# Performance work log

Hardware: AMD Instinct MI355X
Metric: run time of the kernel (lower is better)

Reference implementation:

```python
import jax, jax.numpy as jnp
import numpy as np
from jax import lax

B, BANDS, HW = 128, 30, 15
DIM, NH, NC = 512, 8, 16
EPS = 1e-5

def _ln(x, w, b):
    m = x.mean(-1, keepdims=True)
    v = ((x - m) ** 2).mean(-1, keepdims=True)
    return (x - m) / jnp.sqrt(v + EPS) * w + b

def _bn(x, g, b, m, v):
    # eval-mode BatchNorm2d over NCHW
    inv = g / jnp.sqrt(v + EPS)
    return x * inv[None, :, None, None] + (b - m * inv)[None, :, None, None]

def _conv(x, w, b):
    y = lax.conv_general_dilated(x, w, (1, 1), 'SAME', dimension_numbers=('NCHW', 'OIHW', 'NCHW'))
    return y + b[None, :, None, None]

def _attn(x, qkv_w, qkv_b, proj_w, proj_b):
    Bq, N, C = x.shape
    hd = C // NH
    qkv = (x @ qkv_w.T + qkv_b).reshape(Bq, N, 3, NH, hd).transpose(2, 0, 3, 1, 4)
    q, k, v = qkv[0], qkv[1], qkv[2]
    a = jax.nn.softmax(jnp.einsum('bhnd,bhmd->bhnm', q, k) * (hd ** -0.5), axis=-1)
    o = jnp.einsum('bhnm,bhmd->bhnd', a, v).transpose(0, 2, 1, 3).reshape(Bq, N, C)
    return o @ proj_w.T + proj_b

def _mlp(x, w1, b1, w2, b2):
    return jax.nn.gelu(x @ w1.T + b1, approximate=False) @ w2.T + b2

def _forward(x, conv_h_w, conv_h_b, bn_h_g, bn_h_b, bn_h_m, bn_h_v, cnn_conv_w, cnn_conv_b, cnn_bn_g, cnn_bn_b, cnn_bn_m, cnn_bn_v, cnn_fc_w, cnn_fc_b, spa_cls, spe_cls, spa_pos, spe_pos, blk_n1_w, blk_n1_b, blk_n2_w, blk_n2_b, blk_qkv_w, blk_qkv_b, blk_proj_w, blk_proj_b, blk_fc1_w, blk_fc1_b, blk_fc2_w, blk_fc2_b, norm1_w, norm1_b, norm2_w, norm2_b, head_w, head_b):
    x = x[:, 0]  # squeeze(1) -> [B, BANDS, H, W]
    Bn = x.shape[0]
    # --- spatial stream ---
    h = jax.nn.relu(_bn(_conv(x, conv_h_w, conv_h_b), bn_h_g, bn_h_b, bn_h_m, bn_h_v))
    spa = h.reshape(Bn, DIM, -1).transpose(0, 2, 1)  # b (h w) c
    spa = jnp.concatenate([jnp.broadcast_to(spa_cls, (Bn, 1, DIM)), spa], axis=1) + spa_pos
    # --- spectral stream: per-band CNN batched across bands in one pass ---
    bands = x.reshape(Bn * BANDS, 1, HW, HW)
    f = jax.nn.relu(_bn(_conv(bands, cnn_conv_w, cnn_conv_b), cnn_bn_g, cnn_bn_b, cnn_bn_m, cnn_bn_v))
    f = f.mean(axis=(2, 3))  # adaptive avg pool to 1x1
    f = jax.nn.relu(f @ cnn_fc_w.T + cnn_fc_b).reshape(Bn, BANDS, DIM)
    spe = jnp.concatenate([jnp.broadcast_to(spe_cls, (Bn, 1, DIM)), f], axis=1) + spe_pos
    xs, ys = spa, spe
    for i in range(2):  # CTMF blocks (eval: drop_path/dropout are identity)
        xin = _ln(jnp.concatenate([ys[:, :1], xs[:, 1:]], axis=1), blk_n1_w[i], blk_n1_b[i])
        yin = _ln(jnp.concatenate([xs[:, :1], ys[:, 1:]], axis=1), blk_n1_w[i], blk_n1_b[i])
        x_ = _attn(xin, blk_qkv_w[i], blk_qkv_b[i], blk_proj_w[i], blk_proj_b[i])
        y_ = _attn(yin, blk_qkv_w[i], blk_qkv_b[i], blk_proj_w[i], blk_proj_b[i])
        xs2 = xs + jnp.concatenate([xs[:, :1] + y_[:, :1], x_[:, 1:]], axis=1)
        ys2 = ys + jnp.concatenate([ys[:, :1] + x_[:, :1], y_[:, 1:]], axis=1)
        xs = xs2 + _mlp(_ln(xs2, blk_n2_w[i], blk_n2_b[i]), blk_fc1_w[i], blk_fc1_b[i], blk_fc2_w[i], blk_fc2_b[i])
        ys = ys2 + _mlp(_ln(ys2, blk_n2_w[i], blk_n2_b[i]), blk_fc1_w[i], blk_fc1_b[i], blk_fc2_w[i], blk_fc2_b[i])
    cls = jnp.concatenate([_ln(xs[:, 0], norm1_w, norm1_b), _ln(ys[:, 0], norm2_w, norm2_b)], axis=-1)
    return cls @ head_w.T + head_b

def setup_inputs() -> dict:
    key = jax.random.key(0)
    ks = jax.random.split(key, 32)
    r = lambda i, shape, s=0.02: jax.random.normal(ks[i], shape, dtype=jnp.float32) * s
    Nspa = HW * HW + 1
    Nspe = BANDS + 1
    return {
        'x': jax.random.normal(ks[0], (B, 1, BANDS, HW, HW), dtype=jnp.float32),
        'conv_h_w': r(1, (DIM, BANDS, 3, 3)),
        'conv_h_b': jnp.zeros((DIM,), jnp.float32),
        'bn_h_g': 1.0 + r(2, (DIM,)),
        'bn_h_b': r(3, (DIM,)),
        'bn_h_m': r(4, (DIM,), 0.1),
        'bn_h_v': 0.5 + jax.random.uniform(ks[5], (DIM,), dtype=jnp.float32),
        'cnn_conv_w': r(6, (128, 1, 3, 3), 0.1),
        'cnn_conv_b': jnp.zeros((128,), jnp.float32),
        'cnn_bn_g': 1.0 + r(7, (128,)),
        'cnn_bn_b': r(8, (128,)),
        'cnn_bn_m': r(9, (128,), 0.1),
        'cnn_bn_v': 0.5 + jax.random.uniform(ks[10], (128,), dtype=jnp.float32),
        'cnn_fc_w': r(11, (DIM, 128)),
        'cnn_fc_b': jnp.zeros((DIM,), jnp.float32),
        'spa_cls': jnp.zeros((1, 1, DIM), jnp.float32),
        'spe_cls': jnp.zeros((1, 1, DIM), jnp.float32),
        'spa_pos': r(12, (1, Nspa, DIM)),
        'spe_pos': r(13, (1, Nspe, DIM)),
        'blk_n1_w': jnp.ones((2, DIM), jnp.float32),
        'blk_n1_b': jnp.zeros((2, DIM), jnp.float32),
        'blk_n2_w': jnp.ones((2, DIM), jnp.float32),
        'blk_n2_b': jnp.zeros((2, DIM), jnp.float32),
        'blk_qkv_w': r(14, (2, 3 * DIM, DIM)),
        'blk_qkv_b': jnp.zeros((2, 3 * DIM), jnp.float32),
        'blk_proj_w': r(15, (2, DIM, DIM)),
        'blk_proj_b': jnp.zeros((2, DIM), jnp.float32),
        'blk_fc1_w': r(16, (2, DIM, DIM)),
        'blk_fc1_b': jnp.zeros((2, DIM), jnp.float32),
        'blk_fc2_w': r(17, (2, DIM, DIM)),
        'blk_fc2_b': jnp.zeros((2, DIM), jnp.float32),
        'norm1_w': jnp.ones((DIM,), jnp.float32),
        'norm1_b': jnp.zeros((DIM,), jnp.float32),
        'norm2_w': jnp.ones((DIM,), jnp.float32),
        'norm2_b': jnp.zeros((DIM,), jnp.float32),
        'head_w': r(18, (NC, 2 * DIM)),
        'head_b': jnp.zeros((NC,), jnp.float32),
    }

def reference(x, conv_h_w, conv_h_b, bn_h_g, bn_h_b, bn_h_m, bn_h_v, cnn_conv_w, cnn_conv_b, cnn_bn_g, cnn_bn_b, cnn_bn_m, cnn_bn_v, cnn_fc_w, cnn_fc_b, spa_cls, spe_cls, spa_pos, spe_pos, blk_n1_w, blk_n1_b, blk_n2_w, blk_n2_b, blk_qkv_w, blk_qkv_b, blk_proj_w, blk_proj_b, blk_fc1_w, blk_fc1_b, blk_fc2_w, blk_fc2_b, norm1_w, norm1_b, norm2_w, norm2_b, head_w, head_b):
    return _forward(x, conv_h_w, conv_h_b, bn_h_g, bn_h_b, bn_h_m, bn_h_v, cnn_conv_w, cnn_conv_b, cnn_bn_g, cnn_bn_b, cnn_bn_m, cnn_bn_v, cnn_fc_w, cnn_fc_b, spa_cls, spe_cls, spa_pos, spe_pos, blk_n1_w, blk_n1_b, blk_n2_w, blk_n2_b, blk_qkv_w, blk_qkv_b, blk_proj_w, blk_proj_b, blk_fc1_w, blk_fc1_b, blk_fc2_w, blk_fc2_b, norm1_w, norm1_b, norm2_w, norm2_b, head_w, head_b)
```

## Files before the change

### kernel.cpp

```cpp
#include <hip/hip_runtime.h>
#include <hip/hip_bf16.h>

typedef unsigned short u16;
typedef __attribute__((ext_vector_type(8))) short bf16x8;
typedef __attribute__((ext_vector_type(4))) float f32x4;

#define NB 128
#define BANDS 30
#define HWD 15
#define NPIX 225
#define DIMC 512
#define NHEAD 8
#define HD 64
#define NSPA 226
#define NSPE 31
#define EPSF 1e-5f
#define KCONV 320
#define MXROWS 28928
#define MYROWS 3968
#define M2ROWS 32896

__device__ __forceinline__ float b2f(u16 u) { return __uint_as_float(((unsigned)u) << 16); }
__device__ __forceinline__ u16 f2b(float f) {
  __hip_bfloat16 h = __float2bfloat16(f);
  return *reinterpret_cast<u16*>(&h);
}

#if __has_builtin(__builtin_amdgcn_global_load_lds)
#define HAVE_GLDS 1
__device__ __forceinline__ void gl_lds16(const void* g, void* l) {
  __builtin_amdgcn_global_load_lds((const __attribute__((address_space(1))) void*)g,
                                   (__attribute__((address_space(3))) void*)l, 16, 0, 0);
}
#else
#define HAVE_GLDS 0
#endif

__global__ __launch_bounds__(256) void cvt_k(const float* __restrict__ s, u16* __restrict__ d, int n) {
  for (int i = blockIdx.x * 256 + threadIdx.x; i < n; i += gridDim.x * 256) d[i] = f2b(s[i]);
}

__global__ __launch_bounds__(256) void convw_k(const float* __restrict__ w, u16* __restrict__ d) {
  int i = blockIdx.x * 256 + threadIdx.x;
  if (i >= DIMC * KCONV) return;
  int r = i / KCONV, c = i - r * KCONV;
  d[i] = (c < 270) ? f2b(w[r * 270 + c]) : (u16)0;
}

__global__ __launch_bounds__(256) void bnprep_k(const float* __restrict__ g, const float* __restrict__ bb,
    const float* __restrict__ bm, const float* __restrict__ bv, const float* __restrict__ cb,
    float* __restrict__ sc, float* __restrict__ sh) {
  int n = blockIdx.x * 256 + threadIdx.x;
  if (n < DIMC) {
    float inv = g[n] * rsqrtf(bv[n] + EPSF);
    sc[n] = inv;
    sh[n] = (cb[n] - bm[n]) * inv + bb[n];
  }
}

__global__ __launch_bounds__(256) void im2col_k(const float* __restrict__ x, u16* __restrict__ Ac) {
  int idx = blockIdx.x * 256 + threadIdx.x;
  if (idx >= 28800 * 40) return;
  int m = idx / 40, g = idx - m * 40;
  int b = m / NPIX, p = m - b * NPIX;
  int i = p / 15, j = p - i * 15;
  union { u16 v[8]; uint4 u; } out;
#pragma unroll
  for (int e = 0; e < 8; e++) {
    int c = g * 8 + e;
    float v = 0.f;
    if (c < 270) {
      int band = c / 9, q = c - band * 9;
      int di = q / 3, dj = q - di * 3;
      int ii = i + di - 1, jj = j + dj - 1;
      if ((unsigned)ii < 15u && (unsigned)jj < 15u)
        v = x[((size_t)b * BANDS + band) * NPIX + ii * 15 + jj];
    }
    out.v[e] = f2b(v);
  }
  *reinterpret_cast<uint4*>(Ac + (size_t)m * KCONV + g * 8) = out.u;
}

__global__ __launch_bounds__(256) void cls_init_k(const float* __restrict__ spa_cls,
    const float* __restrict__ spe_cls, const float* __restrict__ spa_pos,
    const float* __restrict__ spe_pos, float* __restrict__ xs, float* __restrict__ ys) {
  int b = blockIdx.x, t = threadIdx.x;
  int d0 = t, d1 = t + 256;
  xs[(size_t)b * NSPA * DIMC + d0] = spa_cls[d0] + spa_pos[d0];
  xs[(size_t)b * NSPA * DIMC + d1] = spa_cls[d1] + spa_pos[d1];
  ys[(size_t)b * NSPE * DIMC + d0] = spe_cls[d0] + spe_pos[d0];
  ys[(size_t)b * NSPE * DIMC + d1] = spe_cls[d1] + spe_pos[d1];
}

__global__ __launch_bounds__(256) void cnn_conv_k(const float* __restrict__ x,
    const float* __restrict__ w, const float* __restrict__ cb, const float* __restrict__ g,
    const float* __restrict__ bb, const float* __restrict__ bm, const float* __restrict__ bv,
    u16* __restrict__ pooled) {
  __shared__ float img[2][NPIX];
  int b0 = blockIdx.x * 2;
  int t = threadIdx.x;
  for (int idx = t; idx < 2 * NPIX; idx += 256) ((float*)img)[idx] = x[(size_t)b0 * NPIX + idx];
  __syncthreads();
  int half = t >> 7, ch = t & 127;
  const float* im = img[half];
  float inv = g[ch] * rsqrtf(bv[ch] + EPSF);
  float beta = bb[ch] - bm[ch] * inv;
  float w9[9];
#pragma unroll
  for (int q = 0; q < 9; q++) w9[q] = w[ch * 9 + q] * inv;
  float bias = cb[ch] * inv + beta;

  float rm[15], rc[15], rp[15];
#pragma unroll
  for (int j = 0; j < 15; j++) { rm[j] = 0.f; rc[j] = im[j]; }
  float sum = 0.f;
  for (int i = 0; i < 15; i++) {
#pragma unroll
    for (int j = 0; j < 15; j++) rp[j] = (i < 14) ? im[(i + 1) * 15 + j] : 0.f;
    float a[15];
#pragma unroll
    for (int j = 0; j < 15; j++) a[j] = fmaf(w9[4], rc[j], bias);
#pragma unroll
    for (int j = 0; j < 15; j++) {
      if (j > 0)  a[j] = fmaf(w9[3], rc[j - 1], a[j]);
      if (j < 14) a[j] = fmaf(w9[5], rc[j + 1], a[j]);
      a[j] = fmaf(w9[1], rm[j], a[j]);
      if (j > 0)  a[j] = fmaf(w9[0], rm[j - 1], a[j]);
      if (j < 14) a[j] = fmaf(w9[2], rm[j + 1], a[j]);
      a[j] = fmaf(w9[7], rp[j], a[j]);
      if (j > 0)  a[j] = fmaf(w9[6], rp[j - 1], a[j]);
      if (j < 14) a[j] = fmaf(w9[8], rp[j + 1], a[j]);
    }
#pragma unroll
    for (int j = 0; j < 15; j++) sum += fmaxf(a[j], 0.f);
#pragma unroll
    for (int j = 0; j < 15; j++) { rm[j] = rc[j]; rc[j] = rp[j]; }
  }
  pooled[(size_t)(b0 + half) * 128 + ch] = f2b(sum * (1.0f / 225.0f));
}

template <int GATHER>
__global__ __launch_bounds__(256) void ln_c_k(const float* __restrict__ xsc,
    const float* __restrict__ w, const float* __restrict__ bprm, u16* __restrict__ out) {
  int row = blockIdx.x;
  const float* src;
  if (GATHER) {
    if (row < MXROWS) {
      int b = row / NSPA, tk = row - b * NSPA;
      src = (tk == 0) ? xsc + ((size_t)MXROWS + (size_t)b * NSPE) * DIMC
                      : xsc + (size_t)row * DIMC;
    } else {
      int ry = row - MXROWS;
      int b = ry / NSPE, tk = ry - b * NSPE;
      src = (tk == 0) ? xsc + (size_t)b * NSPA * DIMC : xsc + (size_t)row * DIMC;
    }
  } else {
    src = xsc + (size_t)row * DIMC;
  }
  int t = threadIdx.x;
  float x0 = src[t], x1 = src[t + 256];
  float s = x0 + x1, sq = x0 * x0 + x1 * x1;
  for (int off = 32; off; off >>= 1) { s += __shfl_down(s, off); sq += __shfl_down(sq, off); }
  __shared__ float sa[4], sb4[4];
  int wid = t >> 6;
  if ((t & 63) == 0) { sa[wid] = s; sb4[wid] = sq; }
  __syncthreads();
  s = sa[0] + sa[1] + sa[2] + sa[3];
  sq = sb4[0] + sb4[1] + sb4[2] + sb4[3];
  float mean = s * (1.0f / 512.0f);
  float var = sq * (1.0f / 512.0f) - mean * mean;
  float rstd = rsqrtf(var + EPSF);
  out[(size_t)row * DIMC + t] = f2b((x0 - mean) * rstd * w[t] + bprm[t]);
  out[(size_t)row * DIMC + t + 256] = f2b((x1 - mean) * rstd * w[t + 256] + bprm[t + 256]);
}

__global__ __launch_bounds__(256) void ln_cls_k(const float* __restrict__ xs,
    const float* __restrict__ ys, const float* __restrict__ w1, const float* __restrict__ b1,
    const float* __restrict__ w2, const float* __restrict__ b2, float* __restrict__ cls) {
  int gb = blockIdx.x;
  int half = gb & 1, b = gb >> 1;
  const float* src = half ? (ys + (size_t)b * NSPE * DIMC) : (xs + (size_t)b * NSPA * DIMC);
  const float* w = half ? w2 : w1;
  const float* bp = half ? b2 : b1;
  int t = threadIdx.x;
  float x0 = src[t], x1 = src[t + 256];
  float s = x0 + x1, sq = x0 * x0 + x1 * x1;
  for (int off = 32; off; off >>= 1) { s += __shfl_down(s, off); sq += __shfl_down(sq, off); }
  __shared__ float sa[4], sb4[4];
  int wid = t >> 6;
  if ((t & 63) == 0) { sa[wid] = s; sb4[wid] = sq; }
  __syncthreads();
  s = sa[0] + sa[1] + sa[2] + sa[3];
  sq = sb4[0] + sb4[1] + sb4[2] + sb4[3];
  float mean = s * (1.0f / 512.0f);
  float var = sq * (1.0f / 512.0f) - mean * mean;
  float rstd = rsqrtf(var + EPSF);
  cls[(size_t)b * 1024 + half * DIMC + t] = (x0 - mean) * rstd * w[t] + bp[t];
  cls[(size_t)b * 1024 + half * DIMC + t + 256] = (x1 - mean) * rstd * w[t + 256] + bp[t + 256];
}

template <int MODE>
__global__ __launch_bounds__(256) void mgemm_k(const u16* __restrict__ A, const u16* __restrict__ Bw,
    const float* __restrict__ bias, float* outf, u16* outb, int M, int N, int K,
    const float* aux0, const float* aux1, const float* aux2) {
  __shared__ u16 As[128 * 64];
  __shared__ u16 Bs[128 * 64];
  const int t = threadIdx.x;
  const int wid = t >> 6, l = t & 63;
  const int wm = wid >> 1, wn = wid & 1;
  const int fr = l & 15, kg = l >> 4;

  const int nx = gridDim.x, nwg = nx * gridDim.y;
  int hlin = blockIdx.y * nx + blockIdx.x;
  int xcd = hlin & 7, j = hlin >> 3;
  int q8 = nwg >> 3, r8 = nwg & 7;
  int L = (xcd < r8 ? xcd * (q8 + 1) : r8 * (q8 + 1) + (xcd - r8) * q8) + j;
  const int n0 = (L % nx) * 128, m0 = (L / nx) * 128;

  const int srow = l >> 3;
  const int sslot = l & 7;

  f32x4 acc[4][4];
#pragma unroll
  for (int i = 0; i < 4; i++)
#pragma unroll
    for (int j2 = 0; j2 < 4; j2++) acc[i][j2] = (f32x4){0.f, 0.f, 0.f, 0.f};

  for (int kq = 0; kq < K; kq += 64) {
#if !HAVE_GLDS
    uint4 ra[4], rb[4];
#pragma unroll
    for (int i = 0; i < 4; i++) {
      int r = wid * 32 + i * 8 + srow;
      int cg = sslot ^ (r & 7);
      ra[i] = *reinterpret_cast<const uint4*>(A + (size_t)(m0 + r) * K + kq + cg * 8);
      rb[i] = *reinterpret_cast<const uint4*>(Bw + (size_t)(n0 + r) * K + kq + cg * 8);
    }
#endif
    __syncthreads();
#if HAVE_GLDS
#pragma unroll
    for (int i = 0; i < 4; i++) {
      int r = wid * 32 + i * 8 + srow;
      int cg = sslot ^ (r & 7);
      gl_lds16(A + (size_t)(m0 + r) * K + kq + cg * 8, &As[(wid * 32 + i * 8) * 64]);
      gl_lds16(Bw + (size_t)(n0 + r) * K + kq + cg * 8, &Bs[(wid * 32 + i * 8) * 64]);
    }
#else
#pragma unroll
    for (int i = 0; i < 4; i++) {
      int r = wid * 32 + i * 8 + srow;
      *reinterpret_cast<uint4*>(&As[r * 64 + sslot * 8]) = ra[i];
      *reinterpret_cast<uint4*>(&Bs[r * 64 + sslot * 8]) = rb[i];
    }
#endif
    __syncthreads();
#pragma unroll
    for (int h = 0; h < 2; h++) {
      bf16x8 af[4], bfr[4];
#pragma unroll
      for (int mi = 0; mi < 4; mi++) {
        int r = wm * 64 + mi * 16 + fr;
        af[mi] = *reinterpret_cast<const bf16x8*>(&As[r * 64 + (((h * 4 + kg) ^ (fr & 7)) * 8)]);
      }
#pragma unroll
      for (int nj = 0; nj < 4; nj++) {
        int n = wn * 64 + nj * 16 + fr;
        bfr[nj] = *reinterpret_cast<const bf16x8*>(&Bs[n * 64 + (((h * 4 + kg) ^ (fr & 7)) * 8)]);
      }
#pragma unroll
      for (int mi = 0; mi < 4; mi++)
#pragma unroll
        for (int nj = 0; nj < 4; nj++)
          acc[mi][nj] = __builtin_amdgcn_mfma_f32_16x16x32_bf16(af[mi], bfr[nj], acc[mi][nj], 0, 0, 0);
    }
  }

#pragma unroll
  for (int mi = 0; mi < 4; mi++) {
#pragma unroll
    for (int q = 0; q < 4; q++) {
      int m = m0 + wm * 64 + mi * 16 + kg * 4 + q;
#pragma unroll
      for (int nj = 0; nj < 4; nj++) {
        int n = n0 + wn * 64 + nj * 16 + fr;
        float v = acc[mi][nj][q];
        if (MODE == 0) {
          outb[(size_t)m * N + n] = f2b(v + bias[n]);
        } else if (MODE == 1) {
          float z = v + bias[n];
          outb[(size_t)m * N + n] = f2b(0.5f * z * (1.0f + erff(z * 0.70710678118f)));
        } else if (MODE == 2) {
          size_t idx = (size_t)m * N + n;
          outf[idx] = v + bias[n] + aux0[idx];
        } else if (MODE == 3) {
          int b = m / NPIX, p = m - b * NPIX;
          float z = fmaxf(v * aux0[n] + aux1[n], 0.f) + aux2[(size_t)(p + 1) * DIMC + n];
          outf[((size_t)b * NSPA + p + 1) * DIMC + n] = z;
        } else if (MODE == 4) {
          int b = m / BANDS, band = m - b * BANDS;
          float z = fmaxf(v + bias[n], 0.f) + aux0[(size_t)(band + 1) * DIMC + n];
          outf[((size_t)b * NSPE + band + 1) * DIMC + n] = z;
        } else if (MODE == 5) {
          float z = v + bias[n];
          int tk, sidx;
          if (m < MXROWS) {
            int b = m / NSPA; tk = m - b * NSPA; sidx = b;
          } else {
            int ry = m - MXROWS; int b = ry / NSPE; tk = ry - b * NSPE; sidx = 128 + b;
          }
          if (tk == 0) outb[(size_t)sidx * DIMC + n] = f2b(z);
          else outf[(size_t)m * N + n] += z;
        }
      }
    }
  }
}

__global__ __launch_bounds__(256) void cls_swap_k(float* __restrict__ xsc,
                                                  const u16* __restrict__ clsprj) {
  int b = blockIdx.x, t = threadIdx.x;
  size_t xrow = (size_t)b * NSPA * DIMC;
  size_t yrow = ((size_t)MXROWS + (size_t)b * NSPE) * DIMC;
#pragma unroll
  for (int q = 0; q < 2; q++) {
    int d = t + q * 256;
    xsc[xrow + d] = 2.0f * xsc[xrow + d] + b2f(clsprj[(size_t)(128 + b) * DIMC + d]);
    xsc[yrow + d] = 2.0f * xsc[yrow + d] + b2f(clsprj[(size_t)b * DIMC + d]);
  }
}

template <int NTOK, int KP>
__global__ __launch_bounds__(256) void vt_k(const u16* __restrict__ qkv, u16* __restrict__ vtout) {
  __shared__ u16 Vl[64 * 72];
  int h = blockIdx.x, b = blockIdx.y;
  int t = threadIdx.x;
  const size_t rs = 3 * DIMC;
  const u16* src = qkv + (size_t)b * NTOK * rs + 2 * DIMC + h * HD;
  u16* dst = vtout + (size_t)(b * NHEAD + h) * HD * KP;
  for (int kt = 0; kt < KP / 64; kt++) {
    __syncthreads();
#pragma unroll
    for (int p = 0; p < 2; p++) {
      int idx = p * 256 + t;
      int row = idx >> 3, c = idx & 7;
      int tok = kt * 64 + row;
      uint4 v = make_uint4(0, 0, 0, 0);
      if (tok < NTOK) v = *reinterpret_cast<const uint4*>(src + (size_t)tok * rs + c * 8);
      *reinterpret_cast<uint4*>(&Vl[row * 72 + c * 8]) = v;
    }
    __syncthreads();
    int d = t & 63, tg = t >> 6;
    unsigned pu[8];
#pragma unroll
    for (int i = 0; i < 8; i++) {
      unsigned a = Vl[(tg * 16 + 2 * i) * 72 + d];
      unsigned bb2 = Vl[(tg * 16 + 2 * i + 1) * 72 + d];
      pu[i] = (bb2 << 16) | a;
    }
    uint4 o0 = make_uint4(pu[0], pu[1], pu[2], pu[3]);
    uint4 o1 = make_uint4(pu[4], pu[5], pu[6], pu[7]);
    u16* dp = dst + (size_t)d * KP + kt * 64 + tg * 16;
    *reinterpret_cast<uint4*>(dp) = o0;
    *reinterpret_cast<uint4*>(dp + 8) = o1;
  }
}

__device__ __forceinline__ int fsw(int row, int chunk) {
  return row * 64 + ((chunk ^ (row & 7)) << 3);
}
__device__ __forceinline__ void stage64(const u16* __restrict__ gsrc, size_t gstride,
                                        u16* lds, int w, int l) {
#pragma unroll
  for (int i = 0; i < 2; i++) {
    int r = w * 16 + i * 8 + (l >> 3);
    int c = l & 7;
    int scg = c ^ (r & 7);
    const u16* g = gsrc + (size_t)r * gstride + scg * 8;
#if HAVE_GLDS
    gl_lds16(g, &lds[(w * 16 + i * 8) * 64]);
#else
    *reinterpret_cast<uint4*>(&lds[r * 64 + c * 8]) = *reinterpret_cast<const uint4*>(g);
#endif
  }
}

__global__ __launch_bounds__(256) void flashm_k(const u16* __restrict__ qkv,
    const u16* __restrict__ vt, u16* __restrict__ o, int N, int kpad, float scale) {
  __shared__ u16 Qs[64 * 64], Ks[64 * 64], Vs[64 * 64];
  __shared__ u16 Ol[64 * 72];
  const int qt = blockIdx.x, h = blockIdx.y, b = blockIdx.z;
  const int t = threadIdx.x;
  const int w = t >> 6, l = t & 63;
  const int lr = l & 15, lk = l >> 4;
  const size_t rs = 3 * DIMC;
  const size_t qbase = (size_t)b * N * rs + h * HD;
  const u16* vbase = vt + (size_t)(b * NHEAD + h) * HD * kpad;

  stage64(qkv + qbase + (size_t)(qt * 64) * rs, rs, Qs, w, l);
  __syncthreads();
  bf16x8 bq0 = *reinterpret_cast<const bf16x8*>(&Qs[fsw(w * 16 + lr, lk)]);
  bf16x8 bq1 = *reinterpret_cast<const bf16x8*>(&Qs[fsw(w * 16 + lr, 4 + lk)]);

  float m_i = -1e30f, l_i = 0.f;
  f32x4 oacc[4];
#pragma unroll
  for (int mi = 0; mi < 4; mi++) oacc[mi] = (f32x4){0.f, 0.f, 0.f, 0.f};

  const int nkt = (kpad + 63) >> 6;
  for (int kt = 0; kt < nkt; kt++) {
    __syncthreads();
    stage64(qkv + qbase + DIMC + (size_t)(kt * 64) * rs, rs, Ks, w, l);
    stage64(vbase + kt * 64, (size_t)kpad, Vs, w, l);
    __syncthreads();

    f32x4 st[4];
#pragma unroll
    for (int mi = 0; mi < 4; mi++) st[mi] = (f32x4){0.f, 0.f, 0.f, 0.f};
#pragma unroll
    for (int mi = 0; mi < 4; mi++) {
      bf16x8 ak0 = *reinterpret_cast<const bf16x8*>(&Ks[fsw(mi * 16 + lr, lk)]);
      bf16x8 ak1 = *reinterpret_cast<const bf16x8*>(&Ks[fsw(mi * 16 + lr, 4 + lk)]);
      st[mi] = __builtin_amdgcn_mfma_f32_16x16x32_bf16(ak0, bq0, st[mi], 0, 0, 0);
      st[mi] = __builtin_amdgcn_mfma_f32_16x16x32_bf16(ak1, bq1, st[mi], 0, 0, 0);
    }

    float sv[4][4];
    float tmax = -1e30f;
#pragma unroll
    for (int mi = 0; mi < 4; mi++)
#pragma unroll
      for (int q = 0; q < 4; q++) {
        int kgl = kt * 64 + mi * 16 + lk * 4 + q;
        float v = (kgl < N) ? st[mi][q] * scale : -1e30f;
        sv[mi][q] = v;
        tmax = fmaxf(tmax, v);
      }
    tmax = fmaxf(tmax, __shfl_xor(tmax, 16));
    tmax = fmaxf(tmax, __shfl_xor(tmax, 32));
    float mn = fmaxf(m_i, tmax);
    float corr = __expf(m_i - mn);
    m_i = mn;
    float rsum = 0.f;
#pragma unroll
    for (int mi = 0; mi < 4; mi++)
#pragma unroll
      for (int q = 0; q < 4; q++) {
        float p = __expf(sv[mi][q] - mn);
        sv[mi][q] = p;
        rsum += p;
      }
    rsum += __shfl_xor(rsum, 16);
    rsum += __shfl_xor(rsum, 32);
    l_i = l_i * corr + rsum;
#pragma unroll
    for (int mi = 0; mi < 4; mi++) oacc[mi] *= corr;

    unsigned pk[4][2];
#pragma unroll
    for (int mi = 0; mi < 4; mi++) {
      pk[mi][0] = ((unsigned)f2b(sv[mi][1]) << 16) | (unsigned)f2b(sv[mi][0]);
      pk[mi][1] = ((unsigned)f2b(sv[mi][3]) << 16) | (unsigned)f2b(sv[mi][2]);
    }
    int src0 = lr + 32 * (lk & 1);
    int src1 = src0 + 16;
    bool hi = lk >= 2;
    bf16x8 pbv[2];
#pragma unroll
    for (int c = 0; c < 2; c++) {
      unsigned a0 = __shfl(pk[2 * c][0], src0), b0 = __shfl(pk[2 * c + 1][0], src0);
      unsigned a1 = __shfl(pk[2 * c][1], src0), b1 = __shfl(pk[2 * c + 1][1], src0);
      unsigned a2 = __shfl(pk[2 * c][0], src1), b2 = __shfl(pk[2 * c + 1][0], src1);
      unsigned a3 = __shfl(pk[2 * c][1], src1), b3 = __shfl(pk[2 * c + 1][1], src1);
      union { unsigned u[4]; bf16x8 v; } pu;
      pu.u[0] = hi ? b0 : a0;
      pu.u[1] = hi ? b1 : a1;
      pu.u[2] = hi ? b2 : a2;
      pu.u[3] = hi ? b3 : a3;
      pbv[c] = pu.v;
    }

#pragma unroll
    for (int mi = 0; mi < 4; mi++) {
      bf16x8 av0 = *reinterpret_cast<const bf16x8*>(&Vs[fsw(mi * 16 + lr, lk)]);
      bf16x8 av1 = *reinterpret_cast<const bf16x8*>(&Vs[fsw(mi * 16 + lr, 4 + lk)]);
      oacc[mi] = __builtin_amdgcn_mfma_f32_16x16x32_bf16(av0, pbv[0], oacc[mi], 0, 0, 0);
      oacc[mi] = __builtin_amdgcn_mfma_f32_16x16x32_bf16(av1, pbv[1], oacc[mi], 0, 0, 0);
    }
  }

  float invl = 1.0f / l_i;
#pragma unroll
  for (int mi = 0; mi < 4; mi++) {
    unsigned lo = ((unsigned)f2b(oacc[mi][1] * invl) << 16) | (unsigned)f2b(oacc[mi][0] * invl);
    unsigned hi2 = ((unsigned)f2b(oacc[mi][3] * invl) << 16) | (unsigned)f2b(oacc[mi][2] * invl);
    uint2 pr; pr.x = lo; pr.y = hi2;
    *reinterpret_cast<uint2*>(&Ol[(w * 16 + lr) * 72 + mi * 16 + lk * 4]) = pr;
  }
  __syncthreads();
  {
    int row = t >> 2, c4 = t & 3;
    int qrow = qt * 64 + row;
    if (qrow < N) {
      uint4 v0 = *reinterpret_cast<const uint4*>(&Ol[row * 72 + c4 * 8]);
      uint4 v1 = *reinterpret_cast<const uint4*>(&Ol[row * 72 + (c4 + 4) * 8]);
      u16* op = o + ((size_t)b * N + qrow) * DIMC + h * HD;
      *reinterpret_cast<uint4*>(op + c4 * 8) = v0;
      *reinterpret_cast<uint4*>(op + (c4 + 4) * 8) = v1;
    }
  }
}

__global__ __launch_bounds__(256) void head_k(const float* __restrict__ cls,
    const float* __restrict__ hw, const float* __restrict__ hb, float* __restrict__ out) {
  __shared__ float cl[1024];
  __shared__ float part[256];
  int b = blockIdx.x, t = threadIdx.x;
  for (int idx = t; idx < 1024; idx += 256) cl[idx] = cls[(size_t)b * 1024 + idx];
  __syncthreads();
  int c = t >> 4, sl = t & 15;
  float p = 0.f;
  for (int j = 0; j < 64; j++) p += cl[sl * 64 + j] * hw[(size_t)c * 1024 + sl * 64 + j];
  part[t] = p;
  __syncthreads();
  if (sl == 0) {
    float sum = hb[c];
    for (int q = 0; q < 16; q++) sum += part[c * 16 + q];
    out[(size_t)b * 16 + c] = sum;
  }
}

extern "C" void kernel_launch(void* const* d_in, const int* in_sizes, int n_in,
                              void* d_out, int out_size, void* d_ws, size_t ws_size,
                              hipStream_t stream) {
  const float* x        = (const float*)d_in[0];
  const float* conv_h_w = (const float*)d_in[1];
  const float* conv_h_b = (const float*)d_in[2];
  const float* bn_h_g   = (const float*)d_in[3];
  const float* bn_h_b   = (const float*)d_in[4];
  const float* bn_h_m   = (const float*)d_in[5];
  const float* bn_h_v   = (const float*)d_in[6];
  const float* cnn_conv_w = (const float*)d_in[7];
  const float* cnn_conv_b = (const float*)d_in[8];
  const float* cnn_bn_g = (const float*)d_in[9];
  const float* cnn_bn_b = (const float*)d_in[10];
  const float* cnn_bn_m = (const float*)d_in[11];
  const float* cnn_bn_v = (const float*)d_in[12];
  const float* cnn_fc_w = (const float*)d_in[13];
  const float* cnn_fc_b = (const float*)d_in[14];
  const float* spa_cls  = (const float*)d_in[15];
  const float* spe_cls  = (const float*)d_in[16];
  const float* spa_pos  = (const float*)d_in[17];
  const float* spe_pos  = (const float*)d_in[18];
  const float* blk_n1_w = (const float*)d_in[19];
  const float* blk_n1_b = (const float*)d_in[20];
  const float* blk_n2_w = (const float*)d_in[21];
  const float* blk_n2_b = (const float*)d_in[22];
  const float* blk_qkv_w = (const float*)d_in[23];
  const float* blk_qkv_b = (const float*)d_in[24];
  const float* blk_proj_w = (const float*)d_in[25];
  const float* blk_proj_b = (const float*)d_in[26];
  const float* blk_fc1_w = (const float*)d_in[27];
  const float* blk_fc1_b = (const float*)d_in[28];
  const float* blk_fc2_w = (const float*)d_in[29];
  const float* blk_fc2_b = (const float*)d_in[30];
  const float* norm1_w  = (const float*)d_in[31];
  const float* norm1_b  = (const float*)d_in[32];
  const float* norm2_w  = (const float*)d_in[33];
  const float* norm2_b  = (const float*)d_in[34];
  const float* head_w   = (const float*)d_in[35];
  const float* head_b   = (const float*)d_in[36];

  char* ws = (char*)d_ws;
  size_t off = 0;
  auto take = [&](size_t bytes) -> char* {
    char* p = ws + off;
    off = (off + bytes + 255) & ~(size_t)255;
    return p;
  };
  const int Mx = MXROWS, M2 = M2ROWS;
  const int Mc = NB * NPIX;
  const int Mf = NB * BANDS;
  float* xsc  = (float*)take((size_t)M2 * DIMC * 4);
  float* ysb  = xsc + (size_t)Mx * DIMC;
  u16* xyin   = (u16*)take((size_t)M2 * DIMC * 2);
  u16* qkvxy  = (u16*)take((size_t)M2 * 3 * DIMC * 2);
  u16* oxy    = (u16*)take((size_t)M2 * DIMC * 2);
  u16* clsprj = (u16*)take((size_t)256 * DIMC * 2);
  float* clsb = (float*)take((size_t)NB * 1024 * 4);
  u16* pooled = (u16*)take((size_t)Mf * 128 * 2);
  u16* qkvWb  = (u16*)take((size_t)2 * 3 * DIMC * DIMC * 2);
  u16* projWb = (u16*)take((size_t)2 * DIMC * DIMC * 2);
  u16* fc1Wb  = (u16*)take((size_t)2 * DIMC * DIMC * 2);
  u16* fc2Wb  = (u16*)take((size_t)2 * DIMC * DIMC * 2);
  u16* fcWb   = (u16*)take((size_t)DIMC * 128 * 2);
  u16* convWb = (u16*)take((size_t)DIMC * KCONV * 2);
  float* bnsc = (float*)take(DIMC * 4);
  float* bnsh = (float*)take(DIMC * 4);
  u16* vty    = (u16*)take((size_t)NB * NHEAD * HD * 64 * 2);
  u16* Acol   = qkvxy;
  u16* vtx    = xyin;

  cvt_k<<<1024, 256, 0, stream>>>(blk_qkv_w, qkvWb, 2 * 3 * DIMC * DIMC);
  cvt_k<<<1024, 256, 0, stream>>>(blk_proj_w, projWb, 2 * DIMC * DIMC);
  cvt_k<<<1024, 256, 0, stream>>>(blk_fc1_w, fc1Wb, 2 * DIMC * DIMC);
  cvt_k<<<1024, 256, 0, stream>>>(blk_fc2_w, fc2Wb, 2 * DIMC * DIMC);
  cvt_k<<<256, 256, 0, stream>>>(cnn_fc_w, fcWb, DIMC * 128);
  convw_k<<<(DIMC * KCONV + 255) / 256, 256, 0, stream>>>(conv_h_w, convWb);
  bnprep_k<<<2, 256, 0, stream>>>(bn_h_g, bn_h_b, bn_h_m, bn_h_v, conv_h_b, bnsc, bnsh);

  cls_init_k<<<NB, 256, 0, stream>>>(spa_cls, spe_cls, spa_pos, spe_pos, xsc, ysb);
  im2col_k<<<(Mc * 40 + 255) / 256, 256, 0, stream>>>(x, Acol);
  mgemm_k<3><<<dim3(4, Mc / 128), 256, 0, stream>>>(Acol, convWb, nullptr, xsc, nullptr,
      Mc, DIMC, KCONV, bnsc, bnsh, spa_pos);
  cnn_conv_k<<<Mf / 2, 256, 0, stream>>>(x, cnn_conv_w, cnn_conv_b, cnn_bn_g, cnn_bn_b,
                                         cnn_bn_m, cnn_bn_v, pooled);
  mgemm_k<4><<<dim3(4, Mf / 128), 256, 0, stream>>>(pooled, fcWb, cnn_fc_b, ysb, nullptr,
      Mf, DIMC, 128, spe_pos, nullptr, nullptr);

  for (int i = 0; i < 2; i++) {
    const float* n1w = blk_n1_w + i * DIMC;
    const float* n1b = blk_n1_b + i * DIMC;
    const float* n2w = blk_n2_w + i * DIMC;
    const float* n2b = blk_n2_b + i * DIMC;
    const u16* qkvW = qkvWb + (size_t)i * 3 * DIMC * DIMC;
    const float* qkvB = blk_qkv_b + (size_t)i * 3 * DIMC;
    const u16* projW = projWb + (size_t)i * DIMC * DIMC;
    const float* projB = blk_proj_b + (size_t)i * DIMC;
    const u16* fc1W = fc1Wb + (size_t)i * DIMC * DIMC;
    const float* fc1B = blk_fc1_b + (size_t)i * DIMC;
    const u16* fc2W = fc2Wb + (size_t)i * DIMC * DIMC;
    const float* fc2B = blk_fc2_b + (size_t)i * DIMC;

    ln_c_k<1><<<M2, 256, 0, stream>>>(xsc, n1w, n1b, xyin);

    mgemm_k<0><<<dim3(12, M2 / 128), 256, 0, stream>>>(xyin, qkvW, qkvB, nullptr, qkvxy,
        M2, 3 * DIMC, DIMC, nullptr, nullptr, nullptr);

    vt_k<NSPA, 256><<<dim3(NHEAD, NB), 256, 0, stream>>>(qkvxy, vtx);
    vt_k<NSPE, 64><<<dim3(NHEAD, NB), 256, 0, stream>>>(qkvxy + (size_t)Mx * 3 * DIMC, vty);

    flashm_k<<<dim3(4, NHEAD, NB), 256, 0, stream>>>(qkvxy, vtx, oxy, NSPA, 256, 0.125f);
    flashm_k<<<dim3(1, NHEAD, NB), 256, 0, stream>>>(qkvxy + (size_t)Mx * 3 * DIMC, vty,
                                                     oxy + (size_t)Mx * DIMC, NSPE, 64, 0.125f);

    mgemm_k<5><<<dim3(4, M2 / 128), 256, 0, stream>>>(oxy, projW, projB, xsc, clsprj,
        M2, DIMC, DIMC, nullptr, nullptr, nullptr);
    cls_swap_k<<<NB, 256, 0, stream>>>(xsc, clsprj);

    ln_c_k<0><<<M2, 256, 0, stream>>>(xsc, n2w, n2b, xyin);
    mgemm_k<1><<<dim3(4, M2 / 128), 256, 0, stream>>>(xyin, fc1W, fc1B, nullptr, qkvxy,
        M2, DIMC, DIMC, nullptr, nullptr, nullptr);
    mgemm_k<2><<<dim3(4, M2 / 128), 256, 0, stream>>>(qkvxy, fc2W, fc2B, xsc, nullptr,
        M2, DIMC, DIMC, xsc, nullptr, nullptr);
  }

  ln_cls_k<<<NB * 2, 256, 0, stream>>>(xsc, ysb, norm1_w, norm1_b, norm2_w, norm2_b, clsb);
  head_k<<<NB, 256, 0, stream>>>(clsb, head_w, head_b, (float*)d_out);
}
```

Before: 872.7 us.

## Share K/V tiles across all query tiles per head and use wave-per-row LayerNorm

A new spatial attention kernel launches one block per (head, batch). Each of the four waves owns a 64-row query tile, so every K/V tile staged in shared memory serves all 256 query rows instead of being reloaded by four separate blocks. LayerNorm now processes one row per wave with vectorized float4 loads, xor-shuffle reductions and 16-byte bf16 stores, which removes the shared-memory reduction and block barrier. The attention change cuts redundant K/V traffic but reduces the grid fourfold and raises register use (oacc[4][4] per wave), which may lower occupancy and latency hiding.

```diff
diff --git a/kernel.cpp b/kernel.cpp
--- a/kernel.cpp
+++ b/kernel.cpp
@@ -140,9 +140,10 @@
 }
 
 template <int GATHER>
-__global__ __launch_bounds__(256) void ln_c_k(const float* __restrict__ xsc,
+__global__ __launch_bounds__(256) void ln_v_k(const float* __restrict__ xsc,
     const float* __restrict__ w, const float* __restrict__ bprm, u16* __restrict__ out) {
-  int row = blockIdx.x;
+  int wid = threadIdx.x >> 6, lane = threadIdx.x & 63;
+  int row = blockIdx.x * 4 + wid;
   const float* src;
   if (GATHER) {
     if (row < MXROWS) {
@@ -157,21 +158,30 @@
   } else {
     src = xsc + (size_t)row * DIMC;
   }
-  int t = threadIdx.x;
-  float x0 = src[t], x1 = src[t + 256];
-  float s = x0 + x1, sq = x0 * x0 + x1 * x1;
-  for (int off = 32; off; off >>= 1) { s += __shfl_down(s, off); sq += __shfl_down(sq, off); }
-  __shared__ float sa[4], sb4[4];
-  int wid = t >> 6;
-  if ((t & 63) == 0) { sa[wid] = s; sb4[wid] = sq; }
-  __syncthreads();
-  s = sa[0] + sa[1] + sa[2] + sa[3];
-  sq = sb4[0] + sb4[1] + sb4[2] + sb4[3];
+  float4 a0 = *reinterpret_cast<const float4*>(src + lane * 8);
+  float4 a1 = *reinterpret_cast<const float4*>(src + lane * 8 + 4);
+  float s = a0.x + a0.y + a0.z + a0.w + a1.x + a1.y + a1.z + a1.w;
+  float sq = a0.x * a0.x + a0.y * a0.y + a0.z * a0.z + a0.w * a0.w +
+             a1.x * a1.x + a1.y * a1.y + a1.z * a1.z + a1.w * a1.w;
+#pragma unroll
+  for (int off = 1; off <= 32; off <<= 1) { s += __shfl_xor(s, off); sq += __shfl_xor(sq, off); }
   float mean = s * (1.0f / 512.0f);
   float var = sq * (1.0f / 512.0f) - mean * mean;
   float rstd = rsqrtf(var + EPSF);
-  out[(size_t)row * DIMC + t] = f2b((x0 - mean) * rstd * w[t] + bprm[t]);
-  out[(size_t)row * DIMC + t + 256] = f2b((x1 - mean) * rstd * w[t + 256] + bprm[t + 256]);
+  float4 w0 = *reinterpret_cast<const float4*>(w + lane * 8);
+  float4 w1 = *reinterpret_cast<const float4*>(w + lane * 8 + 4);
+  float4 b0 = *reinterpret_cast<const float4*>(bprm + lane * 8);
+  float4 b1 = *reinterpret_cast<const float4*>(bprm + lane * 8 + 4);
+  union { u16 v[8]; uint4 u; } r;
+  r.v[0] = f2b((a0.x - mean) * rstd * w0.x + b0.x);
+  r.v[1] = f2b((a0.y - mean) * rstd * w0.y + b0.y);
+  r.v[2] = f2b((a0.z - mean) * rstd * w0.z + b0.z);
+  r.v[3] = f2b((a0.w - mean) * rstd * w0.w + b0.w);
+  r.v[4] = f2b((a1.x - mean) * rstd * w1.x + b1.x);
+  r.v[5] = f2b((a1.y - mean) * rstd * w1.y + b1.y);
+  r.v[6] = f2b((a1.z - mean) * rstd * w1.z + b1.z);
+  r.v[7] = f2b((a1.w - mean) * rstd * w1.w + b1.w);
+  *reinterpret_cast<uint4*>(out + (size_t)row * DIMC + lane * 8) = r.u;
 }
 
 __global__ __launch_bounds__(256) void ln_cls_k(const float* __restrict__ xs,
@@ -382,6 +392,170 @@
 #else
     *reinterpret_cast<uint4*>(&lds[r * 64 + c * 8]) = *reinterpret_cast<const uint4*>(g);
 #endif
+  }
+}
+
+__global__ __launch_bounds__(256) void flashq_k(const u16* __restrict__ qkv,
+    const u16* __restrict__ vt, u16* __restrict__ o, int N, int kpad, float scale) {
+  __shared__ u16 Qs[4][64 * 64];
+  __shared__ u16 KV[2][64 * 64];
+  u16* Ks = KV[0];
+  u16* Vs = KV[1];
+  u16* Ol = KV[0];
+  const int h = blockIdx.x, b = blockIdx.y;
+  const int t = threadIdx.x;
+  const int w = t >> 6, l = t & 63;
+  const int lr = l & 15, lk = l >> 4;
+  const size_t rs = 3 * DIMC;
+  const size_t qbase = (size_t)b * N * rs + h * HD;
+  const u16* vbase = vt + (size_t)(b * NHEAD + h) * HD * kpad;
+
+#pragma unroll
+  for (int i = 0; i < 8; i++) {
+    int r = i * 8 + (l >> 3);
+    int c = l & 7;
+    int scg = c ^ (r & 7);
+    const u16* g = qkv + qbase + (size_t)(w * 64 + r) * rs + scg * 8;
+#if HAVE_GLDS
+    gl_lds16(g, &Qs[w][(i * 8) * 64]);
+#else
+    *reinterpret_cast<uint4*>(&Qs[w][r * 64 + c * 8]) = *reinterpret_cast<const uint4*>(g);
+#endif
+  }
+  __syncthreads();
+  bf16x8 bq[4][2];
+#pragma unroll
+  for (int nj = 0; nj < 4; nj++) {
+    bq[nj][0] = *reinterpret_cast<const bf16x8*>(&Qs[w][fsw(nj * 16 + lr, lk)]);
+    bq[nj][1] = *reinterpret_cast<const bf16x8*>(&Qs[w][fsw(nj * 16 + lr, 4 + lk)]);
+  }
+
+  float m_i[4], l_i[4];
+  f32x4 oacc[4][4];
+#pragma unroll
+  for (int nj = 0; nj < 4; nj++) { m_i[nj] = -1e30f; l_i[nj] = 0.f; }
+#pragma unroll
+  for (int mi = 0; mi < 4; mi++)
+#pragma unroll
+    for (int nj = 0; nj < 4; nj++) oacc[mi][nj] = (f32x4){0.f, 0.f, 0.f, 0.f};
+
+  const int nkt = kpad >> 6;
+  for (int kt = 0; kt < nkt; kt++) {
+    __syncthreads();
+    stage64(qkv + qbase + DIMC + (size_t)(kt * 64) * rs, rs, Ks, w, l);
+    stage64(vbase + kt * 64, (size_t)kpad, Vs, w, l);
+    __syncthreads();
+
+#pragma unroll
+    for (int nj = 0; nj < 4; nj++) {
+      f32x4 st[4];
+#pragma unroll
+      for (int mi = 0; mi < 4; mi++) st[mi] = (f32x4){0.f, 0.f, 0.f, 0.f};
+      __builtin_amdgcn_s_setprio(1);
+#pragma unroll
+      for (int mi = 0; mi < 4; mi++) {
+        bf16x8 ak0 = *reinterpret_cast<const bf16x8*>(&Ks[fsw(mi * 16 + lr, lk)]);
+        bf16x8 ak1 = *reinterpret_cast<const bf16x8*>(&Ks[fsw(mi * 16 + lr, 4 + lk)]);
+        st[mi] = __builtin_amdgcn_mfma_f32_16x16x32_bf16(ak0, bq[nj][0], st[mi], 0, 0, 0);
+        st[mi] = __builtin_amdgcn_mfma_f32_16x16x32_bf16(ak1, bq[nj][1], st[mi], 0, 0, 0);
+      }
+      __builtin_amdgcn_s_setprio(0);
+
+      float sv[4][4];
+      float tmax = -1e30f;
+#pragma unroll
+      for (int mi = 0; mi < 4; mi++)
+#pragma unroll
+        for (int q = 0; q < 4; q++) {
+          int kgl = kt * 64 + mi * 16 + lk * 4 + q;
+          float v = (kgl < N) ? st[mi][q] * scale : -1e30f;
+          sv[mi][q] = v;
+          tmax = fmaxf(tmax, v);
+        }
+      tmax = fmaxf(tmax, __shfl_xor(tmax, 16));
+      tmax = fmaxf(tmax, __shfl_xor(tmax, 32));
+      float mn = fmaxf(m_i[nj], tmax);
+      float corr = __expf(m_i[nj] - mn);
+      m_i[nj] = mn;
+      float rsum = 0.f;
+#pragma unroll
+      for (int mi = 0; mi < 4; mi++)
+#pragma unroll
+        for (int q = 0; q < 4; q++) {
+          float p = __expf(sv[mi][q] - mn);
+          sv[mi][q] = p;
+          rsum += p;
+        }
+      rsum += __shfl_xor(rsum, 16);
+      rsum += __shfl_xor(rsum, 32);
+      l_i[nj] = l_i[nj] * corr + rsum;
+#pragma unroll
+      for (int mi = 0; mi < 4; mi++) oacc[mi][nj] *= corr;
+
+      unsigned pk[4][2];
+#pragma unroll
+      for (int mi = 0; mi < 4; mi++) {
+        pk[mi][0] = ((unsigned)f2b(sv[mi][1]) << 16) | (unsigned)f2b(sv[mi][0]);
+        pk[mi][1] = ((unsigned)f2b(sv[mi][3]) << 16) | (unsigned)f2b(sv[mi][2]);
+      }
+      int src0 = lr + 32 * (lk & 1);
+      int src1 = src0 + 16;
+      bool hi = lk >= 2;
+      bf16x8 pbv[2];
+#pragma unroll
+      for (int c = 0; c < 2; c++) {
+        unsigned a0 = __shfl(pk[2 * c][0], src0), b0 = __shfl(pk[2 * c + 1][0], src0);
+        unsigned a1 = __shfl(pk[2 * c][1], src0), b1 = __shfl(pk[2 * c + 1][1], src0);
+        unsigned a2 = __shfl(pk[2 * c][0], src1), b2 = __shfl(pk[2 * c + 1][0], src1);
+        unsigned a3 = __shfl(pk[2 * c][1], src1), b3 = __shfl(pk[2 * c + 1][1], src1);
+        union { unsigned u[4]; bf16x8 v; } pu;
+        pu.u[0] = hi ? b0 : a0;
+        pu.u[1] = hi ? b1 : a1;
+        pu.u[2] = hi ? b2 : a2;
+        pu.u[3] = hi ? b3 : a3;
+        pbv[c] = pu.v;
+      }
+
+      __builtin_amdgcn_s_setprio(1);
+#pragma unroll
+      for (int mi = 0; mi < 4; mi++) {
+        bf16x8 av0 = *reinterpret_cast<const bf16x8*>(&Vs[fsw(mi * 16 + lr, lk)]);
+        bf16x8 av1 = *reinterpret_cast<const bf16x8*>(&Vs[fsw(mi * 16 + lr, 4 + lk)]);
+        oacc[mi][nj] = __builtin_amdgcn_mfma_f32_16x16x32_bf16(av0, pbv[0], oacc[mi][nj], 0, 0, 0);
+        oacc[mi][nj] = __builtin_amdgcn_mfma_f32_16x16x32_bf16(av1, pbv[1], oacc[mi][nj], 0, 0, 0);
+      }
+      __builtin_amdgcn_s_setprio(0);
+    }
+  }
+
+  float invl[4];
+#pragma unroll
+  for (int nj = 0; nj < 4; nj++) invl[nj] = 1.0f / l_i[nj];
+  for (int pass = 0; pass < 4; pass++) {
+    __syncthreads();
+    if (w == pass) {
+#pragma unroll
+      for (int mi = 0; mi < 4; mi++)
+#pragma unroll
+        for (int nj = 0; nj < 4; nj++) {
+          unsigned lo = ((unsigned)f2b(oacc[mi][nj][1] * invl[nj]) << 16) |
+                        (unsigned)f2b(oacc[mi][nj][0] * invl[nj]);
+          unsigned hi2 = ((unsigned)f2b(oacc[mi][nj][3] * invl[nj]) << 16) |
+                         (unsigned)f2b(oacc[mi][nj][2] * invl[nj]);
+          uint2 pr; pr.x = lo; pr.y = hi2;
+          *reinterpret_cast<uint2*>(&Ol[(nj * 16 + lr) * 72 + mi * 16 + lk * 4]) = pr;
+        }
+    }
+    __syncthreads();
+    int row = t >> 2, c4 = t & 3;
+    int qrow = pass * 64 + row;
+    if (qrow < N) {
+      uint4 v0 = *reinterpret_cast<const uint4*>(&Ol[row * 72 + c4 * 8]);
+      uint4 v1 = *reinterpret_cast<const uint4*>(&Ol[row * 72 + (c4 + 4) * 8]);
+      u16* op = o + ((size_t)b * N + qrow) * DIMC + h * HD;
+      *reinterpret_cast<uint4*>(op + c4 * 8) = v0;
+      *reinterpret_cast<uint4*>(op + (c4 + 4) * 8) = v1;
+    }
   }
 }
 
@@ -632,7 +806,7 @@
     const u16* fc2W = fc2Wb + (size_t)i * DIMC * DIMC;
     const float* fc2B = blk_fc2_b + (size_t)i * DIMC;
 
-    ln_c_k<1><<<M2, 256, 0, stream>>>(xsc, n1w, n1b, xyin);
+    ln_v_k<1><<<M2 / 4, 256, 0, stream>>>(xsc, n1w, n1b, xyin);
 
     mgemm_k<0><<<dim3(12, M2 / 128), 256, 0, stream>>>(xyin, qkvW, qkvB, nullptr, qkvxy,
         M2, 3 * DIMC, DIMC, nullptr, nullptr, nullptr);
@@ -640,7 +814,7 @@
     vt_k<NSPA, 256><<<dim3(NHEAD, NB), 256, 0, stream>>>(qkvxy, vtx);
     vt_k<NSPE, 64><<<dim3(NHEAD, NB), 256, 0, stream>>>(qkvxy + (size_t)Mx * 3 * DIMC, vty);
 
-    flashm_k<<<dim3(4, NHEAD, NB), 256, 0, stream>>>(qkvxy, vtx, oxy, NSPA, 256, 0.125f);
+    flashq_k<<<dim3(NHEAD, NB), 256, 0, stream>>>(qkvxy, vtx, oxy, NSPA, 256, 0.125f);
     flashm_k<<<dim3(1, NHEAD, NB), 256, 0, stream>>>(qkvxy + (size_t)Mx * 3 * DIMC, vty,
                                                      oxy + (size_t)Mx * DIMC, NSPE, 64, 0.125f);
 
@@ -648,7 +822,7 @@
         M2, DIMC, DIMC, nullptr, nullptr, nullptr);
     cls_swap_k<<<NB, 256, 0, stream>>>(xsc, clsprj);
 
-    ln_c_k<0><<<M2, 256, 0, stream>>>(xsc, n2w, n2b, xyin);
+    ln_v_k<0><<<M2 / 4, 256, 0, stream>>>(xsc, n2w, n2b, xyin);
     mgemm_k<1><<<dim3(4, M2 / 128), 256, 0, stream>>>(xyin, fc1W, fc1B, nullptr, qkvxy,
         M2, DIMC, DIMC, nullptr, nullptr, nullptr);
     mgemm_k<2><<<dim3(4, M2 / 128), 256, 0, stream>>>(qkvxy, fc2W, fc2B, xsc, nullptr,
```

Result: faster. 830.7 us (-4.8%).
